# Optimization experiments

Hardware: AMD Instinct MI355X
Metric: run time of the kernel (lower is better)

The kernel has to match this reference:

```python
import jax, jax.numpy as jnp
import numpy as np

N, E, F_IN, H = 10000, 20000, 128, 8
C1, C2 = 512, 256          # per-head channels: head_dim1*8, head_dim2*8
B, OUT = 64, 10            # graphs per batch, output_dim


def _lin(k, fi, fo):
    return (jax.random.normal(k, (fi, fo), jnp.float32) / np.sqrt(fi)).astype(jnp.float32)


def setup_inputs() -> dict:
    key = jax.random.key(0)
    ks = jax.random.split(key, 24)
    inp = {
        "x": jax.random.normal(ks[0], (N, F_IN), jnp.float32),
        "edge_index": jax.random.randint(ks[1], (2, E), 0, N),
        "batch": jnp.sort(jax.random.randint(ks[2], (N,), 0, B)),
        # conv1 (in=F_IN, per-head C1, H heads)
        "Wq1": _lin(ks[3], F_IN, H * C1), "bq1": 0.01 * jax.random.normal(ks[4], (H * C1,)),
        "Wk1": _lin(ks[5], F_IN, H * C1), "bk1": 0.01 * jax.random.normal(ks[6], (H * C1,)),
        "Wv1": _lin(ks[7], F_IN, H * C1), "bv1": 0.01 * jax.random.normal(ks[8], (H * C1,)),
        "Ws1": _lin(ks[9], F_IN, C1), "bs1": 0.01 * jax.random.normal(ks[10], (C1,)),
        # conv2 (in=C1, per-head C2)
        "Wq2": _lin(ks[11], C1, H * C2), "bq2": 0.01 * jax.random.normal(ks[12], (H * C2,)),
        "Wk2": _lin(ks[13], C1, H * C2), "bk2": 0.01 * jax.random.normal(ks[14], (H * C2,)),
        "Wv2": _lin(ks[15], C1, H * C2), "bv2": 0.01 * jax.random.normal(ks[16], (H * C2,)),
        "Ws2": _lin(ks[17], C1, C2), "bs2": 0.01 * jax.random.normal(ks[18], (C2,)),
        # GlobalAttention gate and final fc
        "Wg": _lin(ks[19], C2, 1), "bg": jnp.zeros((1,), jnp.float32),
        "Wf": _lin(ks[20], C2, OUT), "bf": 0.01 * jax.random.normal(ks[21], (OUT,)),
    }
    return inp


def _segment_softmax(alpha, idx, n):
    # numerically-stable softmax over variable-size segments (PyG softmax)
    amax = jax.ops.segment_max(alpha, idx, num_segments=n)
    amax = jnp.where(jnp.isfinite(amax), amax, 0.0)
    e = jnp.exp(alpha - amax[idx])
    denom = jax.ops.segment_sum(e, idx, num_segments=n)
    return e / (denom[idx] + 1e-16)


def _transformer_conv(x, edge_index, Wq, bq, Wk, bk, Wv, bv, Ws, bs, C):
    n = x.shape[0]
    src, dst = edge_index[0], edge_index[1]  # message flows src -> dst
    q = (x @ Wq + bq).reshape(n, H, C)
    k = (x @ Wk + bk).reshape(n, H, C)
    v = (x @ Wv + bv).reshape(n, H, C)
    # per-edge multi-head attention logits [E, H]
    alpha = jnp.einsum('ehc,ehc->eh', q[dst], k[src]) / np.sqrt(C).astype(np.float32)
    a = _segment_softmax(alpha, dst, n)                       # [E, H]
    out = jax.ops.segment_sum(a[:, :, None] * v[src], dst, num_segments=n)  # [N, H, C]
    out = out.mean(axis=1)                                    # concat=False -> head mean
    return out + x @ Ws + bs                                  # root/skip connection


def reference(x, edge_index, batch,
              Wq1, bq1, Wk1, bk1, Wv1, bv1, Ws1, bs1,
              Wq2, bq2, Wk2, bk2, Wv2, bv2, Ws2, bs2,
              Wg, bg, Wf, bf):
    h = jax.nn.elu(_transformer_conv(x, edge_index, Wq1, bq1, Wk1, bk1, Wv1, bv1, Ws1, bs1, C1))
    h = jax.nn.elu(_transformer_conv(h, edge_index, Wq2, bq2, Wk2, bk2, Wv2, bv2, Ws2, bs2, C2))
    # GlobalAttention pooling: gate softmax within each graph, weighted sum
    gate = _segment_softmax((h @ Wg + bg)[:, 0], batch, B)    # [N]
    g = jax.ops.segment_sum(gate[:, None] * h, batch, num_segments=B)  # [B, C2]
    return g @ Wf + bf
```

## Files before the change

kernel.cpp:

```cpp
#include <hip/hip_runtime.h>
#include <math.h>

#define NN 10000
#define NE 20000
#define FIN 128
#define NHEAD 8
#define C1 512
#define C2 256
#define NB 64
#define NOUT 10

typedef _Float16 half8v __attribute__((ext_vector_type(8)));
typedef _Float16 half4v __attribute__((ext_vector_type(4)));
typedef _Float16 half2v __attribute__((ext_vector_type(2)));
typedef float f32x4 __attribute__((ext_vector_type(4)));

template<int VEC> struct VecT;
template<> struct VecT<2> { using T = half2v; };
template<> struct VecT<4> { using T = half4v; };
template<> struct VecT<8> { using T = half8v; };

__device__ __forceinline__ unsigned enc_f(float f) {
    unsigned u = __float_as_uint(f);
    return (u & 0x80000000u) ? ~u : (u | 0x80000000u);
}
__device__ __forceinline__ float dec_f(unsigned e) {
    return (e & 0x80000000u) ? __uint_as_float(e & 0x7fffffffu) : __uint_as_float(~e);
}

__device__ __forceinline__ void gload16(const _Float16* g, _Float16* l) {
    __builtin_amdgcn_global_load_lds(
        (const __attribute__((address_space(1))) unsigned int*)(const void*)g,
        (__attribute__((address_space(3))) unsigned int*)(void*)l, 16, 0, 0);
}

__global__ void cvt_f16(const float* __restrict__ in, _Float16* __restrict__ out, int n) {
    int i = blockIdx.x * blockDim.x + threadIdx.x;
    if (i < n) out[i] = (_Float16)in[i];
}

__global__ void transpose_cvt(const float* __restrict__ W, _Float16* __restrict__ Wt,
                              int K, int N) {
    __shared__ float tile[32][33];
    int n0 = blockIdx.x * 32, k0 = blockIdx.y * 32;
    int tx = threadIdx.x, ty = threadIdx.y;
    for (int j = ty; j < 32; j += 8) tile[j][tx] = W[(size_t)(k0 + j) * N + n0 + tx];
    __syncthreads();
    for (int j = ty; j < 32; j += 8)
        Wt[(size_t)(n0 + j) * K + k0 + tx] = (_Float16)tile[tx][j];
}

__global__ void transpose_stack(const float* __restrict__ Wv, _Float16* __restrict__ Bt,
                                int Cin, int Cout) {
    __shared__ float tile[32][33];
    int h = blockIdx.z;
    int c0 = blockIdx.x * 32, k0 = blockIdx.y * 32;
    int tx = threadIdx.x, ty = threadIdx.y;
    for (int j = ty; j < 32; j += 8)
        tile[j][tx] = Wv[(size_t)(k0 + j) * (NHEAD * Cout) + (size_t)h * Cout + c0 + tx];
    __syncthreads();
    for (int j = ty; j < 32; j += 8)
        Bt[(size_t)(c0 + j) * (NHEAD * Cin) + (size_t)h * Cin + k0 + tx] = (_Float16)tile[tx][j];
}

__global__ void bvmean_k(const float* __restrict__ bv, float* __restrict__ bvm, int C) {
    int c = blockIdx.x * blockDim.x + threadIdx.x;
    if (c >= C) return;
    float s = 0.f;
    #pragma unroll
    for (int h = 0; h < NHEAD; ++h) s += bv[h * C + c];
    bvm[c] = s * (1.0f / NHEAD);
}

__global__ void bcat1_k(const float* __restrict__ bs1, float* __restrict__ o) {
    int i = blockIdx.x * blockDim.x + threadIdx.x;
    if (i < NHEAD * FIN + C1) o[i] = (i < NHEAD * FIN) ? 0.f : bs1[i - NHEAD * FIN];
}
__global__ void bcat2_k(const float* __restrict__ bq2, const float* __restrict__ bk2,
                        const float* __restrict__ bv2, const float* __restrict__ bs2,
                        float* __restrict__ o) {
    int i = blockIdx.x * blockDim.x + threadIdx.x;
    const int n = NHEAD * C2;
    if (i < n) o[i] = bq2[i];
    else if (i < 2 * n) o[i] = bk2[i - n];
    else if (i < 3 * n) o[i] = bv2[i - 2 * n];
    else if (i < 3 * n + C2) o[i] = bs2[i - 3 * n];
}

__global__ void mstack_k(const _Float16* __restrict__ wtq1, const _Float16* __restrict__ wtk1,
                         _Float16* __restrict__ Mst) {
    int h = blockIdx.z;
    int i = blockIdx.x * 16 + threadIdx.x;
    int j = blockIdx.y * 16 + threadIdx.y;
    float acc = 0.f;
    for (int c = 0; c < C1; ++c)
        acc += (float)wtq1[((size_t)h * C1 + c) * FIN + i] *
               (float)wtk1[((size_t)h * C1 + c) * FIN + j];
    Mst[((size_t)h * FIN + j) * FIN + i] = (_Float16)acc;
}

__global__ void uvprep(const float* __restrict__ Wq1, const float* __restrict__ Wk1,
                       const float* __restrict__ bq1, const float* __restrict__ bk1,
                       float* __restrict__ u, float* __restrict__ v, float* __restrict__ ch) {
    int h = blockIdx.x, i = threadIdx.x;
    float su = 0.f, sv = 0.f;
    for (int c = 0; c < C1; ++c) {
        su += Wq1[(size_t)i * (NHEAD * C1) + h * C1 + c] * bk1[h * C1 + c];
        sv += Wk1[(size_t)i * (NHEAD * C1) + h * C1 + c] * bq1[h * C1 + c];
    }
    u[h * FIN + i] = su;
    v[h * FIN + i] = sv;
    if (i == 0) {
        float s = 0.f;
        for (int c = 0; c < C1; ++c) s += bq1[h * C1 + c] * bk1[h * C1 + c];
        ch[h] = s;
    }
}

__global__ void udvs_k(const _Float16* __restrict__ xb, const float* __restrict__ u,
                       const float* __restrict__ v, const float* __restrict__ ch,
                       float* __restrict__ ud, float* __restrict__ vs) {
    int idx = blockIdx.x * blockDim.x + threadIdx.x;
    if (idx >= NN * NHEAD) return;
    int n = idx >> 3, h = idx & 7;
    float su = ch[h], sv = 0.f;
    for (int i = 0; i < FIN; ++i) {
        float xv = (float)xb[(size_t)n * FIN + i];
        su += xv * u[h * FIN + i];
        sv += xv * v[h * FIN + i];
    }
    ud[idx] = su;
    vs[idx] = sv;
}

#define GEMM_BODY                                                                   \
    __shared__ _Float16 As[128 * 32];                                               \
    __shared__ _Float16 Bs[128 * 32];                                               \
    const int t = threadIdx.x;                                                      \
    const int m0 = blockIdx.y * 128, n0 = blockIdx.x * 128;                         \
    const int w = t >> 6, lane = t & 63;                                            \
    const int wr = w >> 1, wc = w & 1;                                              \
    const int r_lo = lane >> 2, slot = lane & 3;                                    \
    f32x4 acc[4][4];                                                                \
    _Pragma("unroll")                                                               \
    for (int m = 0; m < 4; ++m)                                                     \
        _Pragma("unroll")                                                           \
        for (int n = 0; n < 4; ++n)                                                 \
            _Pragma("unroll")                                                       \
            for (int j = 0; j < 4; ++j) acc[m][n][j] = 0.f;                         \
    for (int k0 = 0; k0 < K; k0 += 32) {                                            \
        _Pragma("unroll")                                                           \
        for (int i = 0; i < 2; ++i) {                                               \
            int chunk = 2 * w + i;                                                  \
            int row = chunk * 16 + r_lo;                                            \
            int gr = m0 + row; gr = gr < M ? gr : M - 1;                            \
            gload16(A + (size_t)gr * K + k0 + slot * 8, &As[chunk * 512]);          \
            gload16(Bt + (size_t)(n0 + row) * K + k0 + slot * 8, &Bs[chunk * 512]); \
        }                                                                           \
        __syncthreads();                                                            \
        half8v af[4], bf[4];                                                        \
        _Pragma("unroll")                                                           \
        for (int m = 0; m < 4; ++m)                                                 \
            af[m] = *(const half8v*)(&As[(wr * 64 + m * 16 + (lane & 15)) * 32 + (lane >> 4) * 8]); \
        _Pragma("unroll")                                                           \
        for (int n = 0; n < 4; ++n)                                                 \
            bf[n] = *(const half8v*)(&Bs[(wc * 64 + n * 16 + (lane & 15)) * 32 + (lane >> 4) * 8]); \
        _Pragma("unroll")                                                           \
        for (int m = 0; m < 4; ++m)                                                 \
            _Pragma("unroll")                                                       \
            for (int n = 0; n < 4; ++n)                                             \
                acc[m][n] = __builtin_amdgcn_mfma_f32_16x16x32_f16(af[m], bf[n], acc[m][n], 0, 0, 0); \
        __syncthreads();                                                            \
    }

template<bool OUT_HALF, bool ACCUM>
__global__ __launch_bounds__(256) void gemm_tn(
    const _Float16* __restrict__ A, const _Float16* __restrict__ Bt,
    const float* __restrict__ bias, void* __restrict__ Cout, int ldc,
    int M, int K)
{
    GEMM_BODY
    #pragma unroll
    for (int m = 0; m < 4; ++m) {
        int r0 = m0 + wr * 64 + m * 16 + (lane >> 4) * 4;
        #pragma unroll
        for (int n = 0; n < 4; ++n) {
            int col = n0 + wc * 64 + n * 16 + (lane & 15);
            float b = 0.f;
            if (!ACCUM) b = bias[col];
            #pragma unroll
            for (int r = 0; r < 4; ++r) {
                int row = r0 + r;
                if (row < M) {
                    float v = acc[m][n][r] + b;
                    if (ACCUM) v += ((float*)Cout)[(size_t)row * ldc + col];
                    if (OUT_HALF) ((_Float16*)Cout)[(size_t)row * ldc + col] = (_Float16)v;
                    else          ((float*)Cout)[(size_t)row * ldc + col] = v;
                }
            }
        }
    }
}

__global__ __launch_bounds__(256) void gemm_dual(
    const _Float16* __restrict__ A, const _Float16* __restrict__ Bt,
    const float* __restrict__ bias, _Float16* __restrict__ out16, int ld16,
    float* __restrict__ out32, int ld32, int NSPLIT, int M, int K)
{
    GEMM_BODY
    #pragma unroll
    for (int m = 0; m < 4; ++m) {
        int r0 = m0 + wr * 64 + m * 16 + (lane >> 4) * 4;
        #pragma unroll
        for (int n = 0; n < 4; ++n) {
            int col = n0 + wc * 64 + n * 16 + (lane & 15);
            float b = bias[col];
            #pragma unroll
            for (int r = 0; r < 4; ++r) {
                int row = r0 + r;
                if (row < M) {
                    float v = acc[m][n][r] + b;
                    if (col < NSPLIT) out16[(size_t)row * ld16 + col] = (_Float16)v;
                    else              out32[(size_t)row * ld32 + (col - NSPLIT)] = v;
                }
            }
        }
    }
}

__global__ void zero_i32(int* __restrict__ p, int n) {
    int i = blockIdx.x * blockDim.x + threadIdx.x;
    if (i < n) p[i] = 0;
}
__global__ void hist_dst(const int* __restrict__ dst, int* __restrict__ deg) {
    int e = blockIdx.x * blockDim.x + threadIdx.x;
    if (e < NE) atomicAdd(&deg[dst[e]], 1);
}
__global__ void scan_deg(const int* __restrict__ deg, int* __restrict__ rowptr,
                         int* __restrict__ cursor, int n) {
    __shared__ int s[256];
    __shared__ int carry;
    int t = threadIdx.x;
    if (t == 0) carry = 0;
    __syncthreads();
    for (int base = 0; base < n; base += 256) {
        int v = (base + t < n) ? deg[base + t] : 0;
        s[t] = v;
        __syncthreads();
        for (int off = 1; off < 256; off <<= 1) {
            int x = (t >= off) ? s[t - off] : 0;
            __syncthreads();
            s[t] += x;
            __syncthreads();
        }
        int excl = carry + s[t] - v;
        if (base + t < n) { rowptr[base + t] = excl; cursor[base + t] = excl; }
        __syncthreads();
        if (t == 255) carry += s[255];
        __syncthreads();
    }
    if (t == 0) rowptr[n] = carry;
}
__global__ void scatter_edges(const int* __restrict__ dst, int* __restrict__ cursor,
                              int* __restrict__ eids) {
    int e = blockIdx.x * blockDim.x + threadIdx.x;
    if (e < NE) {
        int pos = atomicAdd(&cursor[dst[e]], 1);
        eids[pos] = e;
    }
}

__global__ void init_seg(unsigned* __restrict__ amax, float* __restrict__ denom, int n) {
    int i = blockIdx.x * blockDim.x + threadIdx.x;
    if (i < n) { amax[i] = 0x007FFFFFu; denom[i] = 0.f; }
}

__global__ void edge_alpha_lr(const _Float16* __restrict__ T, const _Float16* __restrict__ X,
                              const float* __restrict__ ud, const float* __restrict__ vs,
                              const int* __restrict__ src, const int* __restrict__ dst,
                              float* __restrict__ alpha, unsigned* __restrict__ amaxU,
                              float scale)
{
    int gi = blockIdx.x * blockDim.x + threadIdx.x;
    int e = gi >> 6, lane = threadIdx.x & 63;
    if (e >= NE) return;
    int s = src[e], d = dst[e];
    half2v xv = *(const half2v*)(X + (size_t)s * FIN + lane * 2);
    #pragma unroll
    for (int h = 0; h < NHEAD; ++h) {
        half2v tv = *(const half2v*)(T + ((size_t)d * NHEAD + h) * FIN + lane * 2);
        float sum = (float)tv[0] * (float)xv[0] + (float)tv[1] * (float)xv[1];
        #pragma unroll
        for (int off = 32; off; off >>= 1) sum += __shfl_xor(sum, off);
        if (lane == 0) {
            float al = (sum + ud[(size_t)d * NHEAD + h] + vs[(size_t)s * NHEAD + h]) * scale;
            alpha[(size_t)e * NHEAD + h] = al;
            atomicMax(&amaxU[(size_t)d * NHEAD + h], enc_f(al));
        }
    }
}

template<int C, int G>
__global__ void edge_alpha_fu(const _Float16* __restrict__ Q, const _Float16* __restrict__ Kh,
                              int ldq, const int* __restrict__ src, const int* __restrict__ dst,
                              float* __restrict__ alpha, unsigned* __restrict__ amaxU,
                              float scale)
{
    constexpr int VEC = C / 64;
    using vecH = typename VecT<VEC>::T;
    int gi = blockIdx.x * blockDim.x + threadIdx.x;
    int e = gi >> 6, lane = threadIdx.x & 63;
    if (e >= NE) return;
    int s = src[e], d = dst[e];
    const _Float16* qp = Q + (size_t)d * ldq + lane * VEC;
    const _Float16* kp = Kh + (size_t)s * ldq + lane * VEC;
    vecH q[G], k[G];
    #pragma unroll
    for (int h = 0; h < G; ++h) {
        q[h] = *(const vecH*)(qp + h * C);
        k[h] = *(const vecH*)(kp + h * C);
    }
    #pragma unroll
    for (int h = 0; h < G; ++h) {
        float sum = 0.f;
        #pragma unroll
        for (int j = 0; j < VEC; ++j) sum += (float)q[h][j] * (float)k[h][j];
        #pragma unroll
        for (int off = 32; off; off >>= 1) sum += __shfl_xor(sum, off);
        if (lane == 0) {
            float al = sum * scale;
            alpha[(size_t)e * NHEAD + h] = al;
            atomicMax(&amaxU[(size_t)d * NHEAD + h], enc_f(al));
        }
    }
}

__global__ void edge_expsum(const float* __restrict__ alpha, const int* __restrict__ dst,
                            const unsigned* __restrict__ amaxU,
                            float* __restrict__ ev, float* __restrict__ denom)
{
    int i = blockIdx.x * blockDim.x + threadIdx.x;
    if (i >= NE * NHEAD) return;
    int e = i >> 3, h = i & 7;
    int d = dst[e];
    float ex = expf(alpha[i] - dec_f(amaxU[(size_t)d * NHEAD + h]));
    ev[i] = ex;
    atomicAdd(&denom[(size_t)d * NHEAD + h], ex);
}

template<int C, int G>
__global__ void zaccum(const _Float16* __restrict__ X, const float* __restrict__ ev,
                       const float* __restrict__ denom, const int* __restrict__ rowptr,
                       const int* __restrict__ eids, const int* __restrict__ src,
                       _Float16* __restrict__ Z, int hbase)
{
    constexpr int VEC = C / 64;
    using vecH = typename VecT<VEC>::T;
    int gi = blockIdx.x * blockDim.x + threadIdx.x;
    int n = gi >> 6, lane = threadIdx.x & 63;
    if (n >= NN) return;
    int beg = rowptr[n], end = rowptr[n + 1];
    float rd[G];
    #pragma unroll
    for (int h = 0; h < G; ++h)
        rd[h] = (1.0f / NHEAD) / (denom[(size_t)n * NHEAD + hbase + h] + 1e-16f);
    float acc[G][VEC];
    #pragma unroll
    for (int h = 0; h < G; ++h)
        #pragma unroll
        for (int j = 0; j < VEC; ++j) acc[h][j] = 0.f;
    for (int i = beg; i < end; ++i) {
        int e = eids[i];
        int s = src[e];
        vecH xv = *(const vecH*)(X + (size_t)s * C + lane * VEC);
        #pragma unroll
        for (int h = 0; h < G; ++h) {
            float cf = ev[(size_t)e * NHEAD + hbase + h] * rd[h];
            #pragma unroll
            for (int j = 0; j < VEC; ++j) acc[h][j] += cf * (float)xv[j];
        }
    }
    #pragma unroll
    for (int h = 0; h < G; ++h) {
        vecH o;
        #pragma unroll
        for (int j = 0; j < VEC; ++j) o[j] = (_Float16)acc[h][j];
        *(vecH*)(Z + (size_t)n * (G * C) + (size_t)h * C + lane * VEC) = o;
    }
}

template<int C, int G>
__global__ void node_aggr_ilp(const _Float16* __restrict__ V, int ldv,
                              const float* __restrict__ ev, const float* __restrict__ denom,
                              const int* __restrict__ rowptr, const int* __restrict__ eids,
                              const int* __restrict__ src, float* __restrict__ acc)
{
    constexpr int VEC = C / 64;
    using vecH = typename VecT<VEC>::T;
    int gi = blockIdx.x * blockDim.x + threadIdx.x;
    int n = gi >> 6, lane = threadIdx.x & 63;
    if (n >= NN) return;
    int beg = rowptr[n], end = rowptr[n + 1];
    float rd[G];
    #pragma unroll
    for (int h = 0; h < G; ++h)
        rd[h] = (1.0f / NHEAD) / (denom[(size_t)n * NHEAD + h] + 1e-16f);
    float a[VEC];
    #pragma unroll
    for (int j = 0; j < VEC; ++j) a[j] = 0.f;
    for (int i = beg; i < end; ++i) {
        int e = eids[i];
        int s = src[e];
        float cf[G];
        #pragma unroll
        for (int h = 0; h < G; ++h) cf[h] = ev[(size_t)e * NHEAD + h] * rd[h];
        vecH v[G];
        #pragma unroll
        for (int h = 0; h < G; ++h)
            v[h] = *(const vecH*)(V + (size_t)s * ldv + h * C + lane * VEC);
        #pragma unroll
        for (int h = 0; h < G; ++h)
            #pragma unroll
            for (int j = 0; j < VEC; ++j) a[j] += cf[h] * (float)v[h][j];
    }
    float* ap = acc + (size_t)n * C + lane * VEC;
    #pragma unroll
    for (int j = 0; j < VEC; ++j) ap[j] += a[j];
}

__global__ void elu_k(float* __restrict__ x, int n) {
    int i = blockIdx.x * blockDim.x + threadIdx.x;
    if (i < n) { float v = x[i]; x[i] = v > 0.f ? v : expm1f(v); }
}
__global__ void elu_cvt_bias(const float* __restrict__ in, _Float16* __restrict__ out,
                             const float* __restrict__ bvm, const int* __restrict__ deg,
                             int total) {
    int i = blockIdx.x * blockDim.x + threadIdx.x;
    if (i >= total) return;
    int c = i & (C1 - 1), n = i >> 9;
    float v = in[i] + (deg[n] > 0 ? bvm[c] : 0.f);
    v = v > 0.f ? v : expm1f(v);
    out[i] = (_Float16)v;
}

__global__ __launch_bounds__(256) void pool_fused(
    const float* __restrict__ H2, const float* __restrict__ Wg,
    const float* __restrict__ bg, const int* __restrict__ batch,
    const float* __restrict__ Wf, const float* __restrict__ bf,
    float* __restrict__ glogit, float* __restrict__ out)
{
    const int b = blockIdx.x;
    const int t = threadIdx.x, lane = t & 63, w = t >> 6;
    __shared__ int sbeg, send;
    __shared__ float sred[4];
    if (t == 0) {
        int lo = 0, hi = NN;
        while (lo < hi) { int mid = (lo + hi) >> 1; if (batch[mid] < b) lo = mid + 1; else hi = mid; }
        sbeg = lo;
        hi = NN;
        while (lo < hi) { int mid = (lo + hi) >> 1; if (batch[mid] < b + 1) lo = mid + 1; else hi = mid; }
        send = lo;
    }
    __syncthreads();
    const int beg = sbeg, end = send;
    const float bg0 = bg[0];

    float lmax = -INFINITY;
    for (int n = beg + w; n < end; n += 4) {
        float4 h = ((const float4*)(H2 + (size_t)n * C2))[lane];
        float4 wv = ((const float4*)Wg)[lane];
        float sum = h.x * wv.x + h.y * wv.y + h.z * wv.z + h.w * wv.w;
        #pragma unroll
        for (int off = 32; off; off >>= 1) sum += __shfl_xor(sum, off);
        sum += bg0;
        if (lane == 0) glogit[n] = sum;
        lmax = fmaxf(lmax, sum);
    }
    if (lane == 0) sred[w] = lmax;
    __syncthreads();
    float m = fmaxf(fmaxf(sred[0], sred[1]), fmaxf(sred[2], sred[3]));
    if (!isfinite(m)) m = 0.f;
    __syncthreads();

    float ls = 0.f;
    for (int n = beg + t; n < end; n += 256) {
        float e = expf(glogit[n] - m);
        glogit[n] = e;
        ls += e;
    }
    #pragma unroll
    for (int off = 32; off; off >>= 1) ls += __shfl_xor(ls, off);
    if (lane == 0) sred[w] = ls;
    __syncthreads();
    const float denom = sred[0] + sred[1] + sred[2] + sred[3] + 1e-16f;
    __syncthreads();

    float acc = 0.f;
    for (int n = beg; n < end; ++n)
        acc += glogit[n] * H2[(size_t)n * C2 + t];
    const float gc = acc / denom;

    for (int o = 0; o < NOUT; ++o) {
        float p = gc * Wf[t * NOUT + o];
        #pragma unroll
        for (int off = 32; off; off >>= 1) p += __shfl_xor(p, off);
        __syncthreads();
        if (lane == 0) sred[w] = p;
        __syncthreads();
        if (t == 0) out[b * NOUT + o] = sred[0] + sred[1] + sred[2] + sred[3] + bf[o];
    }
}

extern "C" void kernel_launch(void* const* d_in, const int* in_sizes, int n_in,
                              void* d_out, int out_size, void* d_ws, size_t ws_size,
                              hipStream_t stream) {
    (void)in_sizes; (void)n_in; (void)out_size; (void)ws_size;
    const float* x     = (const float*)d_in[0];
    const int*   ei    = (const int*)  d_in[1];
    const int*   batch = (const int*)  d_in[2];
    const float* Wq1 = (const float*)d_in[3];  const float* bq1 = (const float*)d_in[4];
    const float* Wk1 = (const float*)d_in[5];  const float* bk1 = (const float*)d_in[6];
    const float* Wv1 = (const float*)d_in[7];  const float* bv1 = (const float*)d_in[8];
    const float* Ws1 = (const float*)d_in[9];  const float* bs1 = (const float*)d_in[10];
    const float* Wq2 = (const float*)d_in[11]; const float* bq2 = (const float*)d_in[12];
    const float* Wk2 = (const float*)d_in[13]; const float* bk2 = (const float*)d_in[14];
    const float* Wv2 = (const float*)d_in[15]; const float* bv2 = (const float*)d_in[16];
    const float* Ws2 = (const float*)d_in[17]; const float* bs2 = (const float*)d_in[18];
    const float* Wg  = (const float*)d_in[19]; const float* bg  = (const float*)d_in[20];
    const float* Wf  = (const float*)d_in[21]; const float* bf  = (const float*)d_in[22];

    const int* src = ei;
    const int* dst = ei + NE;

    char* base = (char*)d_ws;
    size_t off = 0;
    auto alloc = [&](size_t bytes) -> char* {
        char* p = base + off;
        off = (off + bytes + 255) & ~(size_t)255;
        return p;
    };
    _Float16* xb    = (_Float16*)alloc((size_t)NN * FIN * 2);
    _Float16* wtq1  = (_Float16*)alloc((size_t)NHEAD * C1 * FIN * 2);
    _Float16* wtk1  = (_Float16*)alloc((size_t)NHEAD * C1 * FIN * 2);
    _Float16* bvs1  = (_Float16*)alloc((size_t)C1 * NHEAD * FIN * 2);
    _Float16* wcat1 = (_Float16*)alloc((size_t)(NHEAD * FIN + C1) * FIN * 2);
    _Float16* wcat2 = (_Float16*)alloc((size_t)(3 * NHEAD * C2 + C2) * C1 * 2);
    float* uvecs = (float*)alloc((size_t)NHEAD * FIN * 4);
    float* vvecs = (float*)alloc((size_t)NHEAD * FIN * 4);
    float* chd   = (float*)alloc((size_t)NHEAD * 4);
    float* ud    = (float*)alloc((size_t)NN * NHEAD * 4);
    float* vs    = (float*)alloc((size_t)NN * NHEAD * 4);
    float* bcat1 = (float*)alloc((size_t)(NHEAD * FIN + C1) * 4);
    float* bcat2 = (float*)alloc((size_t)(3 * NHEAD * C2 + C2) * 4);
    float* acc1  = (float*)alloc((size_t)NN * C1 * 4);
    _Float16* h1b = (_Float16*)alloc((size_t)NN * C1 * 2);
    float* alpha = (float*)alloc((size_t)NE * NHEAD * 4);
    float* ev    = (float*)alloc((size_t)NE * NHEAD * 4);
    unsigned* amaxU = (unsigned*)alloc((size_t)NN * NHEAD * 4);
    float* denom = (float*)alloc((size_t)NN * NHEAD * 4);
    int* deg    = (int*)alloc((size_t)NN * 4);
    int* rowptr = (int*)alloc((size_t)(NN + 1) * 4);
    int* cursor = (int*)alloc((size_t)NN * 4);
    int* eids   = (int*)alloc((size_t)NE * 4);
    float* bvm1 = (float*)alloc((size_t)C1 * 4);
    _Float16* Tbuf   = (_Float16*)alloc((size_t)NN * NHEAD * FIN * 2);
    _Float16* QKVbuf = (_Float16*)alloc((size_t)NN * 3 * NHEAD * C2 * 2);
    _Float16* Zbuf = QKVbuf;
    float* acc2 = acc1;
    const int LDQKV = 3 * NHEAD * C2;

    _Float16* Mst  = wcat1;
    _Float16* wts1 = wcat1 + (size_t)NHEAD * FIN * FIN;
    _Float16* wq2t = wcat2;
    _Float16* wk2t = wcat2 + (size_t)NHEAD * C2 * C1;
    _Float16* wv2t = wcat2 + (size_t)2 * NHEAD * C2 * C1;
    _Float16* ws2t = wcat2 + (size_t)3 * NHEAD * C2 * C1;

    const dim3 blk(256);
    const float sc1 = 1.0f / sqrtf((float)C1);
    const float sc2 = 1.0f / sqrtf((float)C2);
    const int edge_blocks = (NE * 64) / 256;
    const int node_blocks = (NN * 64) / 256;
    const int gy = (NN + 127) / 128;

    cvt_f16<<<((size_t)NN * FIN + 255) / 256, blk, 0, stream>>>(x, xb, NN * FIN);
    {
        dim3 tb(32, 8);
        transpose_cvt<<<dim3(NHEAD * C1 / 32, FIN / 32), tb, 0, stream>>>(Wq1, wtq1, FIN, NHEAD * C1);
        transpose_cvt<<<dim3(NHEAD * C1 / 32, FIN / 32), tb, 0, stream>>>(Wk1, wtk1, FIN, NHEAD * C1);
        transpose_stack<<<dim3(C1 / 32, FIN / 32, NHEAD), tb, 0, stream>>>(Wv1, bvs1, FIN, C1);
        transpose_cvt<<<dim3(C1 / 32, FIN / 32),         tb, 0, stream>>>(Ws1, wts1, FIN, C1);
        transpose_cvt<<<dim3(NHEAD * C2 / 32, C1 / 32),  tb, 0, stream>>>(Wq2, wq2t, C1, NHEAD * C2);
        transpose_cvt<<<dim3(NHEAD * C2 / 32, C1 / 32),  tb, 0, stream>>>(Wk2, wk2t, C1, NHEAD * C2);
        transpose_cvt<<<dim3(NHEAD * C2 / 32, C1 / 32),  tb, 0, stream>>>(Wv2, wv2t, C1, NHEAD * C2);
        transpose_cvt<<<dim3(C2 / 32, C1 / 32),          tb, 0, stream>>>(Ws2, ws2t, C1, C2);
    }
    bvmean_k<<<(C1 + 255) / 256, blk, 0, stream>>>(bv1, bvm1, C1);
    mstack_k<<<dim3(FIN / 16, FIN / 16, NHEAD), dim3(16, 16), 0, stream>>>(wtq1, wtk1, Mst);
    uvprep<<<NHEAD, FIN, 0, stream>>>(Wq1, Wk1, bq1, bk1, uvecs, vvecs, chd);
    udvs_k<<<(NN * NHEAD + 255) / 256, blk, 0, stream>>>(xb, uvecs, vvecs, chd, ud, vs);
    bcat1_k<<<(NHEAD * FIN + C1 + 255) / 256, blk, 0, stream>>>(bs1, bcat1);
    bcat2_k<<<(3 * NHEAD * C2 + C2 + 255) / 256, blk, 0, stream>>>(bq2, bk2, bv2, bs2, bcat2);

    zero_i32<<<(NN + 255) / 256, blk, 0, stream>>>(deg, NN);
    hist_dst<<<(NE + 255) / 256, blk, 0, stream>>>(dst, deg);
    scan_deg<<<1, blk, 0, stream>>>(deg, rowptr, cursor, NN);
    scatter_edges<<<(NE + 255) / 256, blk, 0, stream>>>(dst, cursor, eids);

    gemm_dual<<<dim3((NHEAD * FIN + C1) / 128, gy), blk, 0, stream>>>(
        xb, wcat1, bcat1, Tbuf, NHEAD * FIN, acc1, C1, NHEAD * FIN, NN, FIN);
    init_seg<<<(NN * NHEAD + 255) / 256, blk, 0, stream>>>(amaxU, denom, NN * NHEAD);
    edge_alpha_lr<<<edge_blocks, blk, 0, stream>>>(Tbuf, xb, ud, vs, src, dst,
                                                   alpha, amaxU, sc1);
    edge_expsum<<<(NE * NHEAD + 255) / 256, blk, 0, stream>>>(alpha, dst, amaxU, ev, denom);
    zaccum<FIN, NHEAD><<<node_blocks, blk, 0, stream>>>(xb, ev, denom, rowptr, eids, src,
                                                        Zbuf, 0);
    gemm_tn<false, true><<<dim3(C1 / 128, gy), blk, 0, stream>>>(
        Zbuf, bvs1, nullptr, acc1, C1, NN, NHEAD * FIN);
    elu_cvt_bias<<<((size_t)NN * C1 + 255) / 256, blk, 0, stream>>>(
        acc1, h1b, bvm1, deg, NN * C1);

    init_seg<<<(NN * NHEAD + 255) / 256, blk, 0, stream>>>(amaxU, denom, NN * NHEAD);
    gemm_dual<<<dim3((LDQKV + C2) / 128, gy), blk, 0, stream>>>(
        h1b, wcat2, bcat2, QKVbuf, LDQKV, acc2, C2, LDQKV, NN, C1);
    edge_alpha_fu<C2, NHEAD><<<edge_blocks, blk, 0, stream>>>(
        QKVbuf, QKVbuf + NHEAD * C2, LDQKV, src, dst, alpha, amaxU, sc2);
    edge_expsum<<<(NE * NHEAD + 255) / 256, blk, 0, stream>>>(alpha, dst, amaxU, ev, denom);
    node_aggr_ilp<C2, NHEAD><<<node_blocks, blk, 0, stream>>>(
        QKVbuf + 2 * NHEAD * C2, LDQKV, ev, denom, rowptr, eids, src, acc2);
    elu_k<<<((size_t)NN * C2 + 255) / 256, blk, 0, stream>>>(acc2, NN * C2);

    pool_fused<<<NB, blk, 0, stream>>>(acc2, Wg, bg, batch, Wf, bf, alpha, (float*)d_out);
}
```

Baseline: 617.6 us.

## Fuse layer-1 skip GEMM, bias and ELU into the aggregation GEMM; swizzle GEMM grids

The layer-1 skip projection (x·Ws1) moves out of the first dual GEMM and into a concatenated-K GEMM that also consumes the aggregated Z buffer. That GEMM applies the biases and ELU in its epilogue and writes fp16 h1 directly. This removes the fp32 acc1 round trip, the accumulate-read and the separate elu_cvt_bias pass. All GEMMs now launch on a 1D grid with an XCD-aware, stripe-swizzled tile mapping meant to improve L2 reuse across MI355X's chiplets. The cost is a branch in the K loop and a per-element deg lookup in the epilogue.

```diff
diff --git a/kernel.cpp b/kernel.cpp
--- a/kernel.cpp
+++ b/kernel.cpp
@@ -34,6 +34,20 @@
         (__attribute__((address_space(3))) unsigned int*)(void*)l, 16, 0, 0);
 }
 
+__device__ __forceinline__ void swz_map(int nwg, int gx, int SW, int& bx, int& by) {
+    int orig = blockIdx.x;
+    int q = nwg >> 3, r = nwg & 7;
+    int xcd = orig & 7, lid = orig >> 3;
+    int wgid = (xcd < r ? xcd * (q + 1) : r * (q + 1) + (xcd - r) * q) + lid;
+    int gy = nwg / gx;
+    int sh = SW * gy;
+    int stripe = wgid / sh;
+    int rem = wgid - stripe * sh;
+    int byq = rem / SW;
+    by = byq;
+    bx = stripe * SW + (rem - byq * SW);
+}
+
 __global__ void cvt_f16(const float* __restrict__ in, _Float16* __restrict__ out, int n) {
     int i = blockIdx.x * blockDim.x + threadIdx.x;
     if (i < n) out[i] = (_Float16)in[i];
@@ -72,10 +86,6 @@
     bvm[c] = s * (1.0f / NHEAD);
 }
 
-__global__ void bcat1_k(const float* __restrict__ bs1, float* __restrict__ o) {
-    int i = blockIdx.x * blockDim.x + threadIdx.x;
-    if (i < NHEAD * FIN + C1) o[i] = (i < NHEAD * FIN) ? 0.f : bs1[i - NHEAD * FIN];
-}
 __global__ void bcat2_k(const float* __restrict__ bq2, const float* __restrict__ bk2,
                         const float* __restrict__ bv2, const float* __restrict__ bs2,
                         float* __restrict__ o) {
@@ -133,11 +143,10 @@
     vs[idx] = sv;
 }
 
-#define GEMM_BODY                                                                   \
+#define GEMM_CORE                                                                   \
     __shared__ _Float16 As[128 * 32];                                               \
     __shared__ _Float16 Bs[128 * 32];                                               \
     const int t = threadIdx.x;                                                      \
-    const int m0 = blockIdx.y * 128, n0 = blockIdx.x * 128;                         \
     const int w = t >> 6, lane = t & 63;                                            \
     const int wr = w >> 1, wc = w & 1;                                              \
     const int r_lo = lane >> 2, slot = lane & 3;                                    \
@@ -147,15 +156,17 @@
         _Pragma("unroll")                                                           \
         for (int n = 0; n < 4; ++n)                                                 \
             _Pragma("unroll")                                                       \
-            for (int j = 0; j < 4; ++j) acc[m][n][j] = 0.f;                         \
-    for (int k0 = 0; k0 < K; k0 += 32) {                                            \
+            for (int j = 0; j < 4; ++j) acc[m][n][j] = 0.f;
+
+#define GEMM_STEP(APTR, ALD, AKO, BPTR, BLD, BKO)                                   \
+    {                                                                               \
         _Pragma("unroll")                                                           \
         for (int i = 0; i < 2; ++i) {                                               \
             int chunk = 2 * w + i;                                                  \
             int row = chunk * 16 + r_lo;                                            \
             int gr = m0 + row; gr = gr < M ? gr : M - 1;                            \
-            gload16(A + (size_t)gr * K + k0 + slot * 8, &As[chunk * 512]);          \
-            gload16(Bt + (size_t)(n0 + row) * K + k0 + slot * 8, &Bs[chunk * 512]); \
+            gload16(APTR + (size_t)gr * ALD + AKO + slot * 8, &As[chunk * 512]);    \
+            gload16(BPTR + (size_t)(n0 + row) * BLD + BKO + slot * 8, &Bs[chunk * 512]); \
         }                                                                           \
         __syncthreads();                                                            \
         half8v af[4], bf[4];                                                        \
@@ -173,30 +184,26 @@
         __syncthreads();                                                            \
     }
 
-template<bool OUT_HALF, bool ACCUM>
-__global__ __launch_bounds__(256) void gemm_tn(
+__global__ __launch_bounds__(256) void gemm_f16(
     const _Float16* __restrict__ A, const _Float16* __restrict__ Bt,
-    const float* __restrict__ bias, void* __restrict__ Cout, int ldc,
-    int M, int K)
-{
-    GEMM_BODY
+    const float* __restrict__ bias, _Float16* __restrict__ Cout, int ldc,
+    int M, int K, int nwg, int gx, int SW)
+{
+    int bx, by; swz_map(nwg, gx, SW, bx, by);
+    const int m0 = by * 128, n0 = bx * 128;
+    GEMM_CORE
+    for (int k0 = 0; k0 < K; k0 += 32) GEMM_STEP(A, K, k0, Bt, K, k0)
     #pragma unroll
     for (int m = 0; m < 4; ++m) {
         int r0 = m0 + wr * 64 + m * 16 + (lane >> 4) * 4;
         #pragma unroll
         for (int n = 0; n < 4; ++n) {
             int col = n0 + wc * 64 + n * 16 + (lane & 15);
-            float b = 0.f;
-            if (!ACCUM) b = bias[col];
+            float b = bias[col];
             #pragma unroll
             for (int r = 0; r < 4; ++r) {
                 int row = r0 + r;
-                if (row < M) {
-                    float v = acc[m][n][r] + b;
-                    if (ACCUM) v += ((float*)Cout)[(size_t)row * ldc + col];
-                    if (OUT_HALF) ((_Float16*)Cout)[(size_t)row * ldc + col] = (_Float16)v;
-                    else          ((float*)Cout)[(size_t)row * ldc + col] = v;
-                }
+                if (row < M) Cout[(size_t)row * ldc + col] = (_Float16)(acc[m][n][r] + b);
             }
         }
     }
@@ -205,9 +212,13 @@
 __global__ __launch_bounds__(256) void gemm_dual(
     const _Float16* __restrict__ A, const _Float16* __restrict__ Bt,
     const float* __restrict__ bias, _Float16* __restrict__ out16, int ld16,
-    float* __restrict__ out32, int ld32, int NSPLIT, int M, int K)
-{
-    GEMM_BODY
+    float* __restrict__ out32, int ld32, int NSPLIT, int M, int K,
+    int nwg, int gx, int SW)
+{
+    int bx, by; swz_map(nwg, gx, SW, bx, by);
+    const int m0 = by * 128, n0 = bx * 128;
+    GEMM_CORE
+    for (int k0 = 0; k0 < K; k0 += 32) GEMM_STEP(A, K, k0, Bt, K, k0)
     #pragma unroll
     for (int m = 0; m < 4; ++m) {
         int r0 = m0 + wr * 64 + m * 16 + (lane >> 4) * 4;
@@ -222,6 +233,43 @@
                     float v = acc[m][n][r] + b;
                     if (col < NSPLIT) out16[(size_t)row * ld16 + col] = (_Float16)v;
                     else              out32[(size_t)row * ld32 + (col - NSPLIT)] = v;
+                }
+            }
+        }
+    }
+}
+
+__global__ __launch_bounds__(256) void gemm_cat2_elu(
+    const _Float16* __restrict__ A1, int K1,
+    const _Float16* __restrict__ A2, int K2,
+    const _Float16* __restrict__ B1,
+    const _Float16* __restrict__ B2,
+    const float* __restrict__ bs1, const float* __restrict__ bvm1,
+    const int* __restrict__ deg, _Float16* __restrict__ h1b,
+    int M, int nwg, int gx, int SW)
+{
+    int bx, by; swz_map(nwg, gx, SW, bx, by);
+    const int m0 = by * 128, n0 = bx * 128;
+    const int K = K1 + K2;
+    GEMM_CORE
+    for (int k0 = 0; k0 < K; k0 += 32) {
+        if (k0 < K1) GEMM_STEP(A1, K1, k0, B1, K1, k0)
+        else         GEMM_STEP(A2, K2, (k0 - K1), B2, K2, (k0 - K1))
+    }
+    #pragma unroll
+    for (int m = 0; m < 4; ++m) {
+        int r0 = m0 + wr * 64 + m * 16 + (lane >> 4) * 4;
+        #pragma unroll
+        for (int n = 0; n < 4; ++n) {
+            int col = n0 + wc * 64 + n * 16 + (lane & 15);
+            float b = bs1[col], bm = bvm1[col];
+            #pragma unroll
+            for (int r = 0; r < 4; ++r) {
+                int row = r0 + r;
+                if (row < M) {
+                    float v = acc[m][n][r] + b + (deg[row] > 0 ? bm : 0.f);
+                    v = v > 0.f ? v : expm1f(v);
+                    h1b[(size_t)row * C1 + col] = (_Float16)v;
                 }
             }
         }
@@ -431,16 +479,6 @@
 __global__ void elu_k(float* __restrict__ x, int n) {
     int i = blockIdx.x * blockDim.x + threadIdx.x;
     if (i < n) { float v = x[i]; x[i] = v > 0.f ? v : expm1f(v); }
-}
-__global__ void elu_cvt_bias(const float* __restrict__ in, _Float16* __restrict__ out,
-                             const float* __restrict__ bvm, const int* __restrict__ deg,
-                             int total) {
-    int i = blockIdx.x * blockDim.x + threadIdx.x;
-    if (i >= total) return;
-    int c = i & (C1 - 1), n = i >> 9;
-    float v = in[i] + (deg[n] > 0 ? bvm[c] : 0.f);
-    v = v > 0.f ? v : expm1f(v);
-    out[i] = (_Float16)v;
 }
 
 __global__ __launch_bounds__(256) void pool_fused(
@@ -543,16 +581,17 @@
     _Float16* wtq1  = (_Float16*)alloc((size_t)NHEAD * C1 * FIN * 2);
     _Float16* wtk1  = (_Float16*)alloc((size_t)NHEAD * C1 * FIN * 2);
     _Float16* bvs1  = (_Float16*)alloc((size_t)C1 * NHEAD * FIN * 2);
-    _Float16* wcat1 = (_Float16*)alloc((size_t)(NHEAD * FIN + C1) * FIN * 2);
+    _Float16* wts1  = (_Float16*)alloc((size_t)C1 * FIN * 2);
+    _Float16* Mst   = (_Float16*)alloc((size_t)NHEAD * FIN * FIN * 2);
     _Float16* wcat2 = (_Float16*)alloc((size_t)(3 * NHEAD * C2 + C2) * C1 * 2);
     float* uvecs = (float*)alloc((size_t)NHEAD * FIN * 4);
     float* vvecs = (float*)alloc((size_t)NHEAD * FIN * 4);
     float* chd   = (float*)alloc((size_t)NHEAD * 4);
     float* ud    = (float*)alloc((size_t)NN * NHEAD * 4);
     float* vs    = (float*)alloc((size_t)NN * NHEAD * 4);
-    float* bcat1 = (float*)alloc((size_t)(NHEAD * FIN + C1) * 4);
+    float* zbias = (float*)alloc((size_t)NHEAD * FIN * 4);
     float* bcat2 = (float*)alloc((size_t)(3 * NHEAD * C2 + C2) * 4);
-    float* acc1  = (float*)alloc((size_t)NN * C1 * 4);
+    float* acc2  = (float*)alloc((size_t)NN * C2 * 4);
     _Float16* h1b = (_Float16*)alloc((size_t)NN * C1 * 2);
     float* alpha = (float*)alloc((size_t)NE * NHEAD * 4);
     float* ev    = (float*)alloc((size_t)NE * NHEAD * 4);
@@ -566,11 +605,8 @@
     _Float16* Tbuf   = (_Float16*)alloc((size_t)NN * NHEAD * FIN * 2);
     _Float16* QKVbuf = (_Float16*)alloc((size_t)NN * 3 * NHEAD * C2 * 2);
     _Float16* Zbuf = QKVbuf;
-    float* acc2 = acc1;
     const int LDQKV = 3 * NHEAD * C2;
 
-    _Float16* Mst  = wcat1;
-    _Float16* wts1 = wcat1 + (size_t)NHEAD * FIN * FIN;
     _Float16* wq2t = wcat2;
     _Float16* wk2t = wcat2 + (size_t)NHEAD * C2 * C1;
     _Float16* wv2t = wcat2 + (size_t)2 * NHEAD * C2 * C1;
@@ -599,7 +635,7 @@
     mstack_k<<<dim3(FIN / 16, FIN / 16, NHEAD), dim3(16, 16), 0, stream>>>(wtq1, wtk1, Mst);
     uvprep<<<NHEAD, FIN, 0, stream>>>(Wq1, Wk1, bq1, bk1, uvecs, vvecs, chd);
     udvs_k<<<(NN * NHEAD + 255) / 256, blk, 0, stream>>>(xb, uvecs, vvecs, chd, ud, vs);
-    bcat1_k<<<(NHEAD * FIN + C1 + 255) / 256, blk, 0, stream>>>(bs1, bcat1);
+    zero_i32<<<(NHEAD * FIN + 255) / 256, blk, 0, stream>>>((int*)zbias, NHEAD * FIN);
     bcat2_k<<<(3 * NHEAD * C2 + C2 + 255) / 256, blk, 0, stream>>>(bq2, bk2, bv2, bs2, bcat2);
 
     zero_i32<<<(NN + 255) / 256, blk, 0, stream>>>(deg, NN);
@@ -607,22 +643,30 @@
     scan_deg<<<1, blk, 0, stream>>>(deg, rowptr, cursor, NN);
     scatter_edges<<<(NE + 255) / 256, blk, 0, stream>>>(dst, cursor, eids);
 
-    gemm_dual<<<dim3((NHEAD * FIN + C1) / 128, gy), blk, 0, stream>>>(
-        xb, wcat1, bcat1, Tbuf, NHEAD * FIN, acc1, C1, NHEAD * FIN, NN, FIN);
+    {
+        int nwg = 8 * gy;
+        gemm_f16<<<nwg, blk, 0, stream>>>(xb, Mst, zbias, Tbuf, NHEAD * FIN, NN, FIN,
+                                          nwg, 8, 8);
+    }
     init_seg<<<(NN * NHEAD + 255) / 256, blk, 0, stream>>>(amaxU, denom, NN * NHEAD);
     edge_alpha_lr<<<edge_blocks, blk, 0, stream>>>(Tbuf, xb, ud, vs, src, dst,
                                                    alpha, amaxU, sc1);
     edge_expsum<<<(NE * NHEAD + 255) / 256, blk, 0, stream>>>(alpha, dst, amaxU, ev, denom);
     zaccum<FIN, NHEAD><<<node_blocks, blk, 0, stream>>>(xb, ev, denom, rowptr, eids, src,
                                                         Zbuf, 0);
-    gemm_tn<false, true><<<dim3(C1 / 128, gy), blk, 0, stream>>>(
-        Zbuf, bvs1, nullptr, acc1, C1, NN, NHEAD * FIN);
-    elu_cvt_bias<<<((size_t)NN * C1 + 255) / 256, blk, 0, stream>>>(
-        acc1, h1b, bvm1, deg, NN * C1);
+    {
+        int nwg = 4 * gy;
+        gemm_cat2_elu<<<nwg, blk, 0, stream>>>(Zbuf, NHEAD * FIN, xb, FIN,
+                                               bvs1, wts1, bs1, bvm1, deg, h1b,
+                                               NN, nwg, 4, 4);
+    }
 
     init_seg<<<(NN * NHEAD + 255) / 256, blk, 0, stream>>>(amaxU, denom, NN * NHEAD);
-    gemm_dual<<<dim3((LDQKV + C2) / 128, gy), blk, 0, stream>>>(
-        h1b, wcat2, bcat2, QKVbuf, LDQKV, acc2, C2, LDQKV, NN, C1);
+    {
+        int nwg = 50 * gy;
+        gemm_dual<<<nwg, blk, 0, stream>>>(h1b, wcat2, bcat2, QKVbuf, LDQKV,
+                                           acc2, C2, LDQKV, NN, C1, nwg, 50, 25);
+    }
     edge_alpha_fu<C2, NHEAD><<<edge_blocks, blk, 0, stream>>>(
         QKVbuf, QKVbuf + NHEAD * C2, LDQKV, src, dst, alpha, amaxU, sc2);
     edge_expsum<<<(NE * NHEAD + 255) / 256, blk, 0, stream>>>(alpha, dst, amaxU, ev, denom);
```

New measurement: 609.3 us. No clear change (-1.3%).
